# Kernel optimization log

Measured on AMD Instinct MI355X. Metric: run time of the kernel, lower is better.

Reference implementation:

```python
import jax, jax.numpy as jnp
import numpy as np

N_NODES = 100000
N_EDGES = 1600000
D_IN = 64
D_OUT = 64


def setup_inputs() -> dict:
    key = jax.random.key(0)
    k1, k2, k3, k4 = jax.random.split(key, 4)
    x = jax.random.normal(k1, (N_NODES, D_IN), dtype=jnp.float32)
    src = jax.random.randint(k2, (N_EDGES,), 0, N_NODES, dtype=jnp.int32)
    dst = jax.random.randint(k3, (N_EDGES,), 0, N_NODES, dtype=jnp.int32)
    W = jax.random.normal(k4, (D_OUT, D_IN), dtype=jnp.float32) / np.sqrt(D_IN)
    b = jnp.zeros((D_OUT,), dtype=jnp.float32)
    return {"x": x, "src": src, "dst": dst, "W": W, "b": b}


def reference(x, src, dst, W, b):
    # DGL SAGEConv with 'gcn' aggregator:
    #   h_neigh = (sum_{j in N_in(i)} x_j + x_i) / (in_degree(i) + 1)
    #   out     = h_neigh @ W^T + b
    N = x.shape[0]
    # gather source features and scatter-add into destination nodes  [N, D_IN]
    neigh_sum = jax.ops.segment_sum(x[src], dst, num_segments=N)
    deg = jax.ops.segment_sum(jnp.ones_like(dst, dtype=x.dtype), dst, num_segments=N)
    h_neigh = (neigh_sum + x) / (deg + 1.0)[:, None]
    return h_neigh @ W.T + b
```

## Files before the change

### kernel.cpp

```cpp
#include <hip/hip_runtime.h>

#define D 64
#define BSH 6
#define BSZ 64
#define NBMAX 2048
#define STILE 4096
#define CAPB 2048
#define CAP  1536
#define SRTC 2056

typedef unsigned int   uint;
typedef unsigned short ushort_t;
typedef __attribute__((ext_vector_type(8))) short bf16x8;
typedef __attribute__((ext_vector_type(4))) float f32x4;

__device__ __forceinline__ ushort_t f2bf(float f) {
    uint u = __float_as_uint(f);
    u += 0x7FFFu + ((u >> 16) & 1u);
    return (ushort_t)(u >> 16);
}

__global__ __launch_bounds__(256) void k_conv(
    const float4* __restrict__ x4, uint4* __restrict__ xb4,
    int* __restrict__ gcnt, int n8, int nb)
{
    const int tid = threadIdx.x;
    int t = blockIdx.x * 256 + tid;
    if (t < n8) {
        float4 a = x4[t * 2];
        float4 c = x4[t * 2 + 1];
        uint4 o;
        o.x = (uint)f2bf(a.x) | ((uint)f2bf(a.y) << 16);
        o.y = (uint)f2bf(a.z) | ((uint)f2bf(a.w) << 16);
        o.z = (uint)f2bf(c.x) | ((uint)f2bf(c.y) << 16);
        o.w = (uint)f2bf(c.z) | ((uint)f2bf(c.w) << 16);
        xb4[t] = o;
    }
    if (blockIdx.x == 0) {
        if (tid < 8) {
            uint4 z; z.x = z.y = z.z = z.w = 0u;
            xb4[n8 + tid] = z;
        }
        for (int i = tid; i < nb; i += 256) gcnt[i] = 0;
    }
}

__global__ __launch_bounds__(256) void k_scatter1p(
    const int* __restrict__ src, const int* __restrict__ dst,
    int* __restrict__ gcnt, int* __restrict__ packedB,
    int nb, int n_edges)
{
    __shared__ int hist[NBMAX];
    const int tid = threadIdx.x;
    const int blk = blockIdx.x;
    for (int i = tid; i < nb; i += 256) hist[i] = 0;
    __syncthreads();

    const int e0 = blk * STILE;
    const int n4 = n_edges >> 2;
    const int4* src4 = (const int4*)src;
    const int4* dst4 = (const int4*)dst;

#pragma unroll
    for (int k = 0; k < STILE / 1024; ++k) {
        int i4 = (e0 >> 2) + k * 256 + tid;
        if (i4 < n4) {
            int4 d = dst4[i4];
            atomicAdd(&hist[d.x >> BSH], 1);
            atomicAdd(&hist[d.y >> BSH], 1);
            atomicAdd(&hist[d.z >> BSH], 1);
            atomicAdd(&hist[d.w >> BSH], 1);
        }
    }
    if (blk == gridDim.x - 1) {
        for (int e = (n4 << 2) + tid; e < n_edges; e += 256)
            atomicAdd(&hist[dst[e] >> BSH], 1);
    }
    __syncthreads();

    for (int i = tid; i < nb; i += 256) {
        int c = hist[i];
        if (c) hist[i] = atomicAdd(&gcnt[i], c);
    }
    __syncthreads();

#pragma unroll
    for (int k = 0; k < STILE / 1024; ++k) {
        int i4 = (e0 >> 2) + k * 256 + tid;
        if (i4 < n4) {
            int4 sv = src4[i4];
            int4 dv = dst4[i4];
            int b, p;
            b = dv.x >> BSH; p = atomicAdd(&hist[b], 1);
            if (p < CAPB) packedB[(size_t)b * CAPB + p] = sv.x | ((dv.x & (BSZ-1)) << 24);
            b = dv.y >> BSH; p = atomicAdd(&hist[b], 1);
            if (p < CAPB) packedB[(size_t)b * CAPB + p] = sv.y | ((dv.y & (BSZ-1)) << 24);
            b = dv.z >> BSH; p = atomicAdd(&hist[b], 1);
            if (p < CAPB) packedB[(size_t)b * CAPB + p] = sv.z | ((dv.z & (BSZ-1)) << 24);
            b = dv.w >> BSH; p = atomicAdd(&hist[b], 1);
            if (p < CAPB) packedB[(size_t)b * CAPB + p] = sv.w | ((dv.w & (BSZ-1)) << 24);
        }
    }
    if (blk == gridDim.x - 1) {
        for (int e = (n4 << 2) + tid; e < n_edges; e += 256) {
            int b = dst[e] >> BSH;
            int p = atomicAdd(&hist[b], 1);
            if (p < CAPB) packedB[(size_t)b * CAPB + p] = src[e] | ((dst[e] & (BSZ-1)) << 24);
        }
    }
}

__global__ __launch_bounds__(512, 8) void k_aggcsr(
    const int* __restrict__ packedB, const int* __restrict__ gcnt,
    const uint4* __restrict__ xb4, const float* __restrict__ W,
    const float* __restrict__ bvec, float* __restrict__ out, int n_nodes)
{
    __shared__ int raw[CAP];
    __shared__ int srt[SRTC];
    __shared__ ushort_t Wl[64 * 64];
    __shared__ int ldeg[BSZ];
    __shared__ int lofs[BSZ];
    __shared__ int cur[BSZ];

    const int tid = threadIdx.x;
    const int bucket = blockIdx.x;
    const int ebase = bucket * CAPB;
    const int ecnt  = min(gcnt[bucket], CAPB);
    const bool fits = (ecnt <= CAP);
    const uint nmax = (uint)(n_nodes - 1);
    const int zrow = n_nodes;

    {
        const int o = tid >> 3;
        const int j = (tid & 7) * 8;
        const float* wp = W + o * 64 + j;
        float4 wa = *(const float4*)wp;
        float4 wb = *(const float4*)(wp + 4);
        uint4 w4;
        w4.x = (uint)f2bf(wa.x) | ((uint)f2bf(wa.y) << 16);
        w4.y = (uint)f2bf(wa.z) | ((uint)f2bf(wa.w) << 16);
        w4.z = (uint)f2bf(wb.x) | ((uint)f2bf(wb.y) << 16);
        w4.w = (uint)f2bf(wb.z) | ((uint)f2bf(wb.w) << 16);
        *(uint4*)((char*)Wl + o * 128 + ((j * 2) ^ ((o & 7) << 4))) = w4;
    }
    if (tid < BSZ) ldeg[tid] = 0;
    __syncthreads();

    if (fits) {
        for (int i = tid; i < ecnt; i += 512) {
            int pk = packedB[ebase + i];
            raw[i] = pk;
            atomicAdd(&ldeg[((uint)pk) >> 24], 1);
        }
    } else {
        for (int i = tid; i < ecnt; i += 512)
            atomicAdd(&ldeg[((uint)packedB[ebase + i]) >> 24], 1);
    }
    __syncthreads();

    {
        int v = 0;
        if (tid < BSZ) { v = (ldeg[tid] + 3) & ~3; lofs[tid] = v; }
        __syncthreads();
        for (int off = 1; off < BSZ; off <<= 1) {
            int t = (tid < BSZ && tid >= off) ? lofs[tid - off] : 0;
            __syncthreads();
            if (tid < BSZ) lofs[tid] += t;
            __syncthreads();
        }
        if (tid < BSZ) { int e = lofs[tid] - v; lofs[tid] = e; cur[tid] = e; }
    }
    __syncthreads();

    if (fits) {
        for (int i = tid; i < ecnt; i += 512) {
            int pk = raw[i];
            int pos = atomicAdd(&cur[((uint)pk) >> 24], 1);
            srt[pos] = pk & 0x00FFFFFF;
        }
        if (tid < BSZ) {
            int base = lofs[tid] + ldeg[tid];
            int end  = lofs[tid] + ((ldeg[tid] + 3) & ~3);
            for (int i = base; i < end; ++i) srt[i] = zrow;
        }
    }
    __syncthreads();

    const int wave = tid >> 6;
    const int lane = tid & 63;
    const int g    = lane >> 3;
    const int f8   = lane & 7;

#define CVLO(u) __uint_as_float((u) << 16)
#define CVHI(u) __uint_as_float((u) & 0xFFFF0000u)

    const uint4* __restrict__ xbf = xb4 + f8;

    const int nl = wave * 8 + g;
    const int node = (bucket << BSH) + nl;
    const bool valid = (node < n_nodes);
    const int cnt = valid ? ldeg[nl] : 0;
    const int eb  = valid ? lofs[nl] : 0;
    const int pc  = (cnt + 3) & ~3;

    float s0 = 0.f, s1 = 0.f, s2 = 0.f, s3 = 0.f;
    float s4 = 0.f, s5 = 0.f, s6 = 0.f, s7 = 0.f;

    if (fits) {
        for (int i = 0; i < pc; i += 4) {
            uint vv[4];
#pragma unroll
            for (int k = 0; k < 4; ++k) vv[k] = (uint)srt[eb + i + k];
            uint4 A[4];
#pragma unroll
            for (int k = 0; k < 4; ++k)
                A[k] = xbf[(size_t)vv[k] * 8];
#pragma unroll
            for (int k = 0; k < 4; ++k) {
                s0 += CVLO(A[k].x);
                s1 += CVHI(A[k].x);
                s2 += CVLO(A[k].y);
                s3 += CVHI(A[k].y);
                s4 += CVLO(A[k].z);
                s5 += CVHI(A[k].z);
                s6 += CVLO(A[k].w);
                s7 += CVHI(A[k].w);
            }
        }
    } else {
        const int nlm = valid ? nl : -1;
        for (int i = 0; i < ecnt; ++i) {
            int pk = packedB[ebase + i];
            float m0 = ((int)(((uint)pk) >> 24) == nlm) ? 1.0f : 0.0f;
            uint4 A0 = xbf[(size_t)min((uint)(pk & 0x00FFFFFF), nmax) * 8];
            s0 = fmaf(m0, CVLO(A0.x), s0);
            s1 = fmaf(m0, CVHI(A0.x), s1);
            s2 = fmaf(m0, CVLO(A0.y), s2);
            s3 = fmaf(m0, CVHI(A0.y), s3);
            s4 = fmaf(m0, CVLO(A0.z), s4);
            s5 = fmaf(m0, CVHI(A0.z), s5);
            s6 = fmaf(m0, CVLO(A0.w), s6);
            s7 = fmaf(m0, CVHI(A0.w), s7);
        }
    }

    uint4 hreg; hreg.x = hreg.y = hreg.z = hreg.w = 0u;
    if (valid) {
        uint4 xv = xbf[(size_t)node * 8];
        float rinv = 1.0f / (float)(cnt + 1);
        float h0 = (s0 + CVLO(xv.x)) * rinv;
        float h1 = (s1 + CVHI(xv.x)) * rinv;
        float h2 = (s2 + CVLO(xv.y)) * rinv;
        float h3 = (s3 + CVHI(xv.y)) * rinv;
        float h4 = (s4 + CVLO(xv.z)) * rinv;
        float h5 = (s5 + CVHI(xv.z)) * rinv;
        float h6 = (s6 + CVLO(xv.w)) * rinv;
        float h7 = (s7 + CVHI(xv.w)) * rinv;
        hreg.x = (uint)f2bf(h0) | ((uint)f2bf(h1) << 16);
        hreg.y = (uint)f2bf(h2) | ((uint)f2bf(h3) << 16);
        hreg.z = (uint)f2bf(h4) | ((uint)f2bf(h5) << 16);
        hreg.w = (uint)f2bf(h6) | ((uint)f2bf(h7) << 16);
    }
#undef CVLO
#undef CVHI

    __syncthreads();

    char* hstage = (char*)srt;
    *(uint4*)(hstage + nl * 128 + ((f8 * 16) ^ ((nl & 7) << 4))) = hreg;
    __syncthreads();

    if (wave < 4) {
        char* hwb = hstage + wave * 2048;
        const int m  = lane & 15;
        const int kg = lane >> 4;
        bf16x8 a0 = *(const bf16x8*)(hwb + m * 128 + (((kg * 16)     ) ^ ((m & 7) << 4)));
        bf16x8 a1 = *(const bf16x8*)(hwb + m * 128 + (((64 + kg * 16)) ^ ((m & 7) << 4)));

        const int node0 = (bucket << BSH) + wave * 16;
#pragma unroll
        for (int c = 0; c < 4; ++c) {
            const int o = c * 16 + m;
            bf16x8 b0 = *(const bf16x8*)((char*)Wl + o * 128 + (((kg * 16)     ) ^ ((o & 7) << 4)));
            bf16x8 b1 = *(const bf16x8*)((char*)Wl + o * 128 + (((64 + kg * 16)) ^ ((o & 7) << 4)));
            f32x4 acc = {0.f, 0.f, 0.f, 0.f};
            acc = __builtin_amdgcn_mfma_f32_16x16x32_bf16(a0, b0, acc, 0, 0, 0);
            acc = __builtin_amdgcn_mfma_f32_16x16x32_bf16(a1, b1, acc, 0, 0, 0);
            const float bias = bvec[o];
#pragma unroll
            for (int r = 0; r < 4; ++r) {
                int row = node0 + kg * 4 + r;
                if (row < n_nodes)
                    out[(size_t)row * 64 + o] = acc[r] + bias;
            }
        }
    }
}

extern "C" void kernel_launch(void* const* d_in, const int* in_sizes, int n_in,
                              void* d_out, int out_size, void* d_ws, size_t ws_size,
                              hipStream_t stream)
{
    const float* x   = (const float*)d_in[0];
    const int*   src = (const int*)d_in[1];
    const int*   dst = (const int*)d_in[2];
    const float* W   = (const float*)d_in[3];
    const float* b   = (const float*)d_in[4];
    float* out = (float*)d_out;

    const int n_nodes = in_sizes[0] / D;
    const int n_edges = in_sizes[1];
    const int nb  = (n_nodes + BSZ - 1) >> BSH;
    const int nbS = (n_edges + STILE - 1) / STILE;

    ushort_t* xb = (ushort_t*)d_ws;
    int* gcnt    = (int*)(xb + (size_t)(n_nodes + 1) * D);
    int* packedB = gcnt + NBMAX;

    const int n8 = n_nodes * D / 8;
    k_conv     <<<(n8 + 255) / 256, 256, 0, stream>>>((const float4*)x, (uint4*)xb,
                                                      gcnt, n8, nb);
    k_scatter1p<<<nbS, 256, 0, stream>>>(src, dst, gcnt, packedB, nb, n_edges);
    k_aggcsr   <<<nb,  512, 0, stream>>>(packedB, gcnt, (const uint4*)xb,
                                         W, b, out, n_nodes);
}
```

Baseline: 77.48 us.

## Fuse bf16 conversion into edge bucketing kernel with larger edge tiles

Merges the fp32-to-bf16 feature conversion and the edge bucket scatter into one 512-thread kernel with a fixed grid, each block converting a slice of x before bucketing its edge tile. The edge tile grows from 4096 to 16384 edges, so fewer blocks do more work and make fewer global atomic reservations. Bucket counters are now cleared with a memset instead of inside the conversion kernel. This saves a launch and overlaps conversion with scatter, but gives the scatter phase far fewer blocks (about 98), which may reduce latency hiding on a large GPU.

```diff
diff --git a/kernel.cpp b/kernel.cpp
--- a/kernel.cpp
+++ b/kernel.cpp
@@ -4,7 +4,7 @@
 #define BSH 6
 #define BSZ 64
 #define NBMAX 2048
-#define STILE 4096
+#define STILE 16384
 #define CAPB 2048
 #define CAP  1536
 #define SRTC 2056
@@ -20,40 +20,40 @@
     return (ushort_t)(u >> 16);
 }
 
-__global__ __launch_bounds__(256) void k_conv(
+__global__ __launch_bounds__(512) void k_scatconv(
     const float4* __restrict__ x4, uint4* __restrict__ xb4,
-    int* __restrict__ gcnt, int n8, int nb)
-{
-    const int tid = threadIdx.x;
-    int t = blockIdx.x * 256 + tid;
-    if (t < n8) {
-        float4 a = x4[t * 2];
-        float4 c = x4[t * 2 + 1];
-        uint4 o;
-        o.x = (uint)f2bf(a.x) | ((uint)f2bf(a.y) << 16);
-        o.y = (uint)f2bf(a.z) | ((uint)f2bf(a.w) << 16);
-        o.z = (uint)f2bf(c.x) | ((uint)f2bf(c.y) << 16);
-        o.w = (uint)f2bf(c.z) | ((uint)f2bf(c.w) << 16);
-        xb4[t] = o;
-    }
-    if (blockIdx.x == 0) {
-        if (tid < 8) {
-            uint4 z; z.x = z.y = z.z = z.w = 0u;
-            xb4[n8 + tid] = z;
-        }
-        for (int i = tid; i < nb; i += 256) gcnt[i] = 0;
-    }
-}
-
-__global__ __launch_bounds__(256) void k_scatter1p(
     const int* __restrict__ src, const int* __restrict__ dst,
     int* __restrict__ gcnt, int* __restrict__ packedB,
-    int nb, int n_edges)
+    int n8, int nb, int nbS, int n_edges)
 {
     __shared__ int hist[NBMAX];
     const int tid = threadIdx.x;
     const int blk = blockIdx.x;
-    for (int i = tid; i < nb; i += 256) hist[i] = 0;
+
+    if (blk == 0 && tid < 8) {
+        uint4 z; z.x = z.y = z.z = z.w = 0u;
+        xb4[n8 + tid] = z;
+    }
+
+    {
+        const int chunk = (n8 + gridDim.x - 1) / gridDim.x;
+        const int lo = blk * chunk;
+        const int hi = min(n8, lo + chunk);
+        for (int t = lo + tid; t < hi; t += 512) {
+            float4 a = x4[t * 2];
+            float4 c = x4[t * 2 + 1];
+            uint4 o;
+            o.x = (uint)f2bf(a.x) | ((uint)f2bf(a.y) << 16);
+            o.y = (uint)f2bf(a.z) | ((uint)f2bf(a.w) << 16);
+            o.z = (uint)f2bf(c.x) | ((uint)f2bf(c.y) << 16);
+            o.w = (uint)f2bf(c.z) | ((uint)f2bf(c.w) << 16);
+            xb4[t] = o;
+        }
+    }
+
+    if (blk >= nbS) return;
+
+    for (int i = tid; i < nb; i += 512) hist[i] = 0;
     __syncthreads();
 
     const int e0 = blk * STILE;
@@ -62,8 +62,8 @@
     const int4* dst4 = (const int4*)dst;
 
 #pragma unroll
-    for (int k = 0; k < STILE / 1024; ++k) {
-        int i4 = (e0 >> 2) + k * 256 + tid;
+    for (int k = 0; k < STILE / 2048; ++k) {
+        int i4 = (e0 >> 2) + k * 512 + tid;
         if (i4 < n4) {
             int4 d = dst4[i4];
             atomicAdd(&hist[d.x >> BSH], 1);
@@ -72,21 +72,21 @@
             atomicAdd(&hist[d.w >> BSH], 1);
         }
     }
-    if (blk == gridDim.x - 1) {
-        for (int e = (n4 << 2) + tid; e < n_edges; e += 256)
+    if (blk == nbS - 1) {
+        for (int e = (n4 << 2) + tid; e < n_edges; e += 512)
             atomicAdd(&hist[dst[e] >> BSH], 1);
     }
     __syncthreads();
 
-    for (int i = tid; i < nb; i += 256) {
+    for (int i = tid; i < nb; i += 512) {
         int c = hist[i];
         if (c) hist[i] = atomicAdd(&gcnt[i], c);
     }
     __syncthreads();
 
 #pragma unroll
-    for (int k = 0; k < STILE / 1024; ++k) {
-        int i4 = (e0 >> 2) + k * 256 + tid;
+    for (int k = 0; k < STILE / 2048; ++k) {
+        int i4 = (e0 >> 2) + k * 512 + tid;
         if (i4 < n4) {
             int4 sv = src4[i4];
             int4 dv = dst4[i4];
@@ -101,8 +101,8 @@
             if (p < CAPB) packedB[(size_t)b * CAPB + p] = sv.w | ((dv.w & (BSZ-1)) << 24);
         }
     }
-    if (blk == gridDim.x - 1) {
-        for (int e = (n4 << 2) + tid; e < n_edges; e += 256) {
+    if (blk == nbS - 1) {
+        for (int e = (n4 << 2) + tid; e < n_edges; e += 512) {
             int b = dst[e] >> BSH;
             int p = atomicAdd(&hist[b], 1);
             if (p < CAPB) packedB[(size_t)b * CAPB + p] = src[e] | ((dst[e] & (BSZ-1)) << 24);
@@ -317,10 +317,13 @@
     int* gcnt    = (int*)(xb + (size_t)(n_nodes + 1) * D);
     int* packedB = gcnt + NBMAX;
 
+    hipMemsetAsync(gcnt, 0, NBMAX * sizeof(int), stream);
+
     const int n8 = n_nodes * D / 8;
-    k_conv     <<<(n8 + 255) / 256, 256, 0, stream>>>((const float4*)x, (uint4*)xb,
-                                                      gcnt, n8, nb);
-    k_scatter1p<<<nbS, 256, 0, stream>>>(src, dst, gcnt, packedB, nb, n_edges);
-    k_aggcsr   <<<nb,  512, 0, stream>>>(packedB, gcnt, (const uint4*)xb,
-                                         W, b, out, n_nodes);
+    const int gridS = 391;
+    k_scatconv<<<gridS, 512, 0, stream>>>((const float4*)x, (uint4*)xb,
+                                          src, dst, gcnt, packedB,
+                                          n8, nb, nbS, n_edges);
+    k_aggcsr  <<<nb,  512, 0, stream>>>(packedB, gcnt, (const uint4*)xb,
+                                        W, b, out, n_nodes);
 }
```

Measured after the change: 74.54 us. 3.8% less time.
